# Performance work log

Measured on AMD Instinct MI355X. Metric: run time of the kernel, lower is better.

The kernel has to match this reference:

```python
import jax, jax.numpy as jnp
import numpy as np

B, S, D_IN, D_OUT = 4, 4096, 512, 512


def setup_inputs() -> dict:
    key = jax.random.key(0)
    k1, k2, k3, k4 = jax.random.split(key, 4)
    sc = 1.0 / np.sqrt(D_IN)
    return {
        "x": jax.random.normal(k1, (B, S, D_IN), dtype=jnp.float32),
        "Wq": jax.random.normal(k2, (D_OUT, D_IN), dtype=jnp.float32) * sc,
        "Wk": jax.random.normal(k3, (D_OUT, D_IN), dtype=jnp.float32) * sc,
        "Wv": jax.random.normal(k4, (D_OUT, D_IN), dtype=jnp.float32) * sc,
    }


def reference(x, Wq, Wk, Wv):
    # nn.Linear: y = x @ W.T  (no bias)
    q = jnp.einsum("bsd,ed->bse", x, Wq)  # [B,S,D_OUT]
    k = jnp.einsum("bsd,ed->bse", x, Wk)
    v = jnp.einsum("bsd,ed->bse", x, Wv)
    scale = 1.0 / jnp.sqrt(jnp.asarray(k.shape[-1], dtype=x.dtype))
    scores = jnp.einsum("bqe,bke->bqk", q, k) * scale  # [B,S,S]
    # causal mask: position q attends to k <= q
    s = x.shape[1]
    causal = jnp.tril(jnp.ones((s, s), dtype=bool))
    scores = jnp.where(causal[None, :, :], scores, -jnp.inf)
    attn = jax.nn.softmax(scores, axis=-1)
    # dropout p=0.0 -> identity
    return jnp.einsum("bqk,bke->bqe", attn, v)  # [B,S,D_OUT]
```

## Files before the change

kernel.cpp:

```cpp
#include <hip/hip_runtime.h>

typedef __attribute__((ext_vector_type(8))) short short8;
typedef __attribute__((ext_vector_type(4))) float f32x4;

#define GLD_AS1 const __attribute__((address_space(1))) void*
#define GLD_AS3 __attribute__((address_space(3))) void*

__device__ __forceinline__ unsigned short f2bf(float f) {
  unsigned u = __builtin_bit_cast(unsigned, f);
  u += 0x7fffu + ((u >> 16) & 1u);
  return (unsigned short)(u >> 16);
}
__device__ __forceinline__ float bf2f(unsigned short h) {
  return __builtin_bit_cast(float, (unsigned)h << 16);
}

__global__ void cvt_f32_bf16(const float* __restrict__ in, unsigned short* __restrict__ out, int n4) {
  int i = blockIdx.x * blockDim.x + threadIdx.x;
  const int st = gridDim.x * blockDim.x;
  for (; i < n4; i += st) {
    float4 f = reinterpret_cast<const float4*>(in)[i];
    unsigned long long p = (unsigned long long)f2bf(f.x)
        | ((unsigned long long)f2bf(f.y) << 16)
        | ((unsigned long long)f2bf(f.z) << 32)
        | ((unsigned long long)f2bf(f.w) << 48);
    reinterpret_cast<unsigned long long*>(out)[i] = p;
  }
}

__global__ void cvt_w3(const float* __restrict__ wq, const float* __restrict__ wk,
                       const float* __restrict__ wv, unsigned short* __restrict__ wcat) {
  const int n4 = 3 * 65536;
  int i = blockIdx.x * blockDim.x + threadIdx.x;
  const int st = gridDim.x * blockDim.x;
  for (; i < n4; i += st) {
    const int seg = i >> 16, off = i & 65535;
    const float* src = (seg == 0) ? wq : (seg == 1) ? wk : wv;
    float4 f = reinterpret_cast<const float4*>(src)[off];
    unsigned long long p = (unsigned long long)f2bf(f.x)
        | ((unsigned long long)f2bf(f.y) << 16)
        | ((unsigned long long)f2bf(f.z) << 32)
        | ((unsigned long long)f2bf(f.w) << 48);
    reinterpret_cast<unsigned long long*>(wcat)[i] = p;
  }
}

__global__ __launch_bounds__(256) void qkv_gemm(
    const unsigned short* __restrict__ xb, const unsigned short* __restrict__ wcat,
    unsigned short* __restrict__ qb, unsigned short* __restrict__ kb,
    unsigned short* __restrict__ vtb) {
  __shared__ unsigned short As[128 * 64];
  __shared__ unsigned short Bs[128 * 64];
  const int tid = threadIdx.x, lane = tid & 63, w = tid >> 6;
  const int m0 = blockIdx.y * 128, n0 = blockIdx.x * 128;
  const int wr = w >> 1, wc = w & 1;
  const float QSCALE = 0.0637587085f;

  f32x4 acc[4][4];
  const f32x4 z4 = {0.f, 0.f, 0.f, 0.f};
  #pragma unroll
  for (int a = 0; a < 4; ++a)
    #pragma unroll
    for (int c = 0; c < 4; ++c) acc[a][c] = z4;

  for (int it = 0; it < 8; ++it) {
    const int k0 = it * 64;
    #pragma unroll
    for (int c = 0; c < 4; ++c) {
      const int rbase = 32 * w + 8 * c;
      const int r = rbase + (lane >> 3);
      const int c16 = (lane & 7) ^ (r & 7);
      const unsigned short* ga = xb + (size_t)(m0 + r) * 512 + k0 + c16 * 8;
      const unsigned short* gb = wcat + (size_t)(n0 + r) * 512 + k0 + c16 * 8;
      __builtin_amdgcn_global_load_lds((GLD_AS1)ga, (GLD_AS3)&As[rbase * 64], 16, 0, 0);
      __builtin_amdgcn_global_load_lds((GLD_AS1)gb, (GLD_AS3)&Bs[rbase * 64], 16, 0, 0);
    }
    __syncthreads();
    #pragma unroll
    for (int ks = 0; ks < 2; ++ks) {
      const int ck = ks * 4 + (lane >> 4);
      short8 av[4], bv[4];
      #pragma unroll
      for (int fr = 0; fr < 4; ++fr) {
        const int rl = 64 * wr + 16 * fr + (lane & 15);
        av[fr] = *reinterpret_cast<const short8*>(&As[rl * 64 + ((ck ^ (rl & 7)) << 3)]);
      }
      #pragma unroll
      for (int fc = 0; fc < 4; ++fc) {
        const int rl = 64 * wc + 16 * fc + (lane & 15);
        bv[fc] = *reinterpret_cast<const short8*>(&Bs[rl * 64 + ((ck ^ (rl & 7)) << 3)]);
      }
      #pragma unroll
      for (int fr = 0; fr < 4; ++fr)
        #pragma unroll
        for (int fc = 0; fc < 4; ++fc)
          acc[fr][fc] = __builtin_amdgcn_mfma_f32_16x16x32_bf16(av[fr], bv[fc], acc[fr][fc], 0, 0, 0);
    }
    __syncthreads();
  }

  const int which = n0 >> 9;
  #pragma unroll
  for (int fr = 0; fr < 4; ++fr) {
    #pragma unroll
    for (int fc = 0; fc < 4; ++fc) {
      const int n = n0 + 64 * wc + 16 * fc + (lane & 15);
      const int nl = n & 511;
      #pragma unroll
      for (int j = 0; j < 4; ++j) {
        const int m = m0 + 64 * wr + 16 * fr + (lane >> 4) * 4 + j;
        const float a = acc[fr][fc][j];
        const unsigned short v = f2bf(which == 0 ? a * QSCALE : a);
        if (which == 0)      qb[(size_t)m * 512 + nl] = v;
        else if (which == 1) kb[(size_t)m * 512 + nl] = v;
        else                 vtb[((size_t)((m >> 12) * 512 + nl)) * 4096 + (m & 4095)] = v;
      }
    }
  }
}

#define FENCE() __builtin_amdgcn_sched_barrier(0)
#define BAR_VM8()  do { FENCE(); asm volatile("s_waitcnt vmcnt(8) lgkmcnt(0)" ::: "memory"); \
                        FENCE(); __builtin_amdgcn_s_barrier(); FENCE(); } while (0)
#define BAR_VM0()  do { FENCE(); asm volatile("s_waitcnt vmcnt(0) lgkmcnt(0)" ::: "memory"); \
                        FENCE(); __builtin_amdgcn_s_barrier(); FENCE(); } while (0)

__global__ __launch_bounds__(512, 2) void attn_fwd(
    const unsigned short* __restrict__ qg, const unsigned short* __restrict__ kg,
    const unsigned short* __restrict__ vtg,
    float* __restrict__ out0,
    unsigned short* __restrict__ out1,
    float* __restrict__ ml) {
  __shared__ __align__(16) unsigned short Ks[2][64 * 512];
  __shared__ __align__(16) unsigned short P_lds[2][64][72];
  __shared__ __align__(16) float psums[2][64];

  const int tid = threadIdx.x, lane = tid & 63, w = tid >> 6;
  const int idx = blockIdx.x;
  const int qt = 63 - (idx >> 3);
  const int b = (idx >> 1) & 3;
  const int half = idx & 1;
  const int nkt = qt + 1;
  const int kt0 = half ? (nkt >> 1) : 0;
  const int kt1 = half ? nkt : (nkt >> 1);
  const int q0 = qt * 64;

  const unsigned short* Qb  = qg  + (size_t)b * 4096 * 512;
  const unsigned short* Kb  = kg  + (size_t)b * 4096 * 512;
  const unsigned short* Vtb = vtg + (size_t)b * 512 * 4096;

  const int wr = w & 3, wc = w >> 2, g = lane >> 4, dw = w * 64;
  const int rbase = 16 * wr + 4 * g;

  short8 qreg[16];
  {
    const unsigned short* qrow = Qb + (size_t)(q0 + 16 * wr + (lane & 15)) * 512 + (lane >> 4) * 8;
    #pragma unroll
    for (int ks = 0; ks < 16; ++ks)
      qreg[ks] = *reinterpret_cast<const short8*>(qrow + ks * 32);
  }

  const f32x4 z4 = {0.f, 0.f, 0.f, 0.f};
  f32x4 oacc[4][4];
  #pragma unroll
  for (int fr = 0; fr < 4; ++fr)
    #pragma unroll
    for (int fc = 0; fc < 4; ++fc) oacc[fr][fc] = z4;

  float l_run[4];
  #pragma unroll
  for (int j = 0; j < 4; ++j) l_run[j] = 0.f;

  short8 vreg[2][4];
  f32x4 sacc_cur[2], sacc_nxt[2];

#define STAGE_K(kt_) do {                                                                \
    _Pragma("unroll")                                                                    \
    for (int r8 = 0; r8 < 8; ++r8) {                                                     \
      const int r_ = r8 * 8 + w;                                                         \
      const unsigned short* g_ = Kb + (size_t)((kt_) * 64 + r_) * 512 + (lane ^ (r_ & 7)) * 8; \
      __builtin_amdgcn_global_load_lds((GLD_AS1)g_, (GLD_AS3)&Ks[(kt_) & 1][r_ * 512], 16, 0, 0); \
    }                                                                                    \
  } while (0)

#define QK_TILE(buf_, S_) do {                                                           \
    _Pragma("unroll")                                                                    \
    for (int ks = 0; ks < 16; ++ks) {                                                    \
      const int ck = ks * 4 + (lane >> 4);                                               \
      _Pragma("unroll")                                                                  \
      for (int fc = 0; fc < 2; ++fc) {                                                   \
        const int rl = 32 * wc + 16 * fc + (lane & 15);                                  \
        const short8 bv = *reinterpret_cast<const short8*>(                              \
            &Ks[buf_][rl * 512 + ((ck ^ (rl & 7)) << 3)]);                               \
        S_[fc] = __builtin_amdgcn_mfma_f32_16x16x32_bf16(qreg[ks], bv, S_[fc], 0, 0, 0); \
      }                                                                                  \
    }                                                                                    \
  } while (0)

#define PV_STEP(pb_) do {                                                                \
    _Pragma("unroll")                                                                    \
    for (int ks = 0; ks < 2; ++ks) {                                                     \
      short8 av[4];                                                                      \
      _Pragma("unroll")                                                                  \
      for (int fr = 0; fr < 4; ++fr)                                                     \
        av[fr] = *reinterpret_cast<const short8*>(                                       \
            &P_lds[pb_][16 * fr + (lane & 15)][ks * 32 + (lane >> 4) * 8]);              \
      __builtin_amdgcn_s_setprio(1);                                                     \
      _Pragma("unroll")                                                                  \
      for (int fr = 0; fr < 4; ++fr)                                                     \
        _Pragma("unroll")                                                                \
        for (int fc = 0; fc < 4; ++fc)                                                   \
          oacc[fr][fc] = __builtin_amdgcn_mfma_f32_16x16x32_bf16(av[fr], vreg[ks][fc],   \
                                                                 oacc[fr][fc], 0, 0, 0);\
      __builtin_amdgcn_s_setprio(0);                                                     \
    }                                                                                    \
  } while (0)

  if (kt0 < kt1) {
    STAGE_K(kt0);
    const bool two = (kt0 + 1 < kt1);
    if (two) STAGE_K(kt0 + 1);
    FENCE();
    if (two) { asm volatile("s_waitcnt vmcnt(8)" ::: "memory"); }
    else     { asm volatile("s_waitcnt vmcnt(0)" ::: "memory"); }
    FENCE();
    __builtin_amdgcn_s_barrier();
    FENCE();
    sacc_cur[0] = z4; sacc_cur[1] = z4;
    QK_TILE(kt0 & 1, sacc_cur);
    BAR_VM0();

    for (int t = kt0; t < kt1; ++t) {
      if (t + 2 < kt1) STAGE_K(t + 2);
      FENCE();
      if (t > kt0) PV_STEP((t - 1) & 1);
      if (t == qt) {
        #pragma unroll
        for (int fc = 0; fc < 2; ++fc) {
          const int col = 32 * wc + 16 * fc + (lane & 15);
          #pragma unroll
          for (int j = 0; j < 4; ++j)
            if (col > rbase + j) sacc_cur[fc][j] = -1e30f;
        }
      }
      {
        const int colb = 32 * wc + (lane & 15);
        #pragma unroll
        for (int j = 0; j < 4; ++j) {
          const float p0 = __builtin_amdgcn_exp2f(sacc_cur[0][j]);
          const float p1 = __builtin_amdgcn_exp2f(sacc_cur[1][j]);
          l_run[j] += p0 + p1;
          P_lds[t & 1][rbase + j][colb]      = f2bf(p0);
          P_lds[t & 1][rbase + j][colb + 16] = f2bf(p1);
        }
      }
      const int kv0 = t * 64;
      #pragma unroll
      for (int ks = 0; ks < 2; ++ks)
        #pragma unroll
        for (int fc = 0; fc < 4; ++fc)
          vreg[ks][fc] = *reinterpret_cast<const short8*>(
              Vtb + (size_t)(dw + 16 * fc + (lane & 15)) * 4096 + kv0 + ks * 32 + (lane >> 4) * 8);
      if (t + 1 < kt1) {
        sacc_nxt[0] = z4; sacc_nxt[1] = z4;
        __builtin_amdgcn_s_setprio(1);
        QK_TILE((t + 1) & 1, sacc_nxt);
        __builtin_amdgcn_s_setprio(0);
        sacc_cur[0] = sacc_nxt[0]; sacc_cur[1] = sacc_nxt[1];
      }
      BAR_VM8();
    }
    PV_STEP((kt1 - 1) & 1);
  }

  #pragma unroll
  for (int j = 0; j < 4; ++j) {
    l_run[j] += __shfl_xor(l_run[j], 1);
    l_run[j] += __shfl_xor(l_run[j], 2);
    l_run[j] += __shfl_xor(l_run[j], 4);
    l_run[j] += __shfl_xor(l_run[j], 8);
  }
  if ((lane & 15) == 0) {
    f32x4 l4 = {l_run[0], l_run[1], l_run[2], l_run[3]};
    *reinterpret_cast<f32x4*>(&psums[wc][rbase]) = l4;
  }
  __syncthreads();
  if ((lane & 15) == 0 && wc == 0) {
    const int rg = b * 4096 + q0 + rbase;
    const f32x4 la = *reinterpret_cast<const f32x4*>(&psums[0][rbase]);
    const f32x4 lb = *reinterpret_cast<const f32x4*>(&psums[1][rbase]);
    f32x4 m4 = {0.f, 0.f, 0.f, 0.f};
    f32x4 l4 = {la[0] + lb[0], la[1] + lb[1], la[2] + lb[2], la[3] + lb[3]};
    *reinterpret_cast<f32x4*>(&ml[(half * 2) * 16384 + rg])     = m4;
    *reinterpret_cast<f32x4*>(&ml[(half * 2 + 1) * 16384 + rg]) = l4;
  }
  if (half == 0) {
    float* ob = out0 + (size_t)b * 4096 * 512;
    #pragma unroll
    for (int fr = 0; fr < 4; ++fr)
      #pragma unroll
      for (int j = 0; j < 4; ++j) {
        const int row = 16 * fr + (lane >> 4) * 4 + j;
        #pragma unroll
        for (int fc = 0; fc < 4; ++fc)
          ob[(size_t)(q0 + row) * 512 + dw + 16 * fc + (lane & 15)] = oacc[fr][fc][j];
      }
  } else {
    unsigned short* ob = out1 + (size_t)b * 4096 * 512;
    #pragma unroll
    for (int fr = 0; fr < 4; ++fr)
      #pragma unroll
      for (int j = 0; j < 4; ++j) {
        const int row = 16 * fr + (lane >> 4) * 4 + j;
        #pragma unroll
        for (int fc = 0; fc < 4; ++fc)
          ob[(size_t)(q0 + row) * 512 + dw + 16 * fc + (lane & 15)] = f2bf(oacc[fr][fc][j]);
      }
  }
#undef STAGE_K
#undef QK_TILE
#undef PV_STEP
}

__global__ void attn_merge(float* __restrict__ out, const unsigned short* __restrict__ o1,
                           const float* __restrict__ ml) {
  const int total = 16384 * 128;
  int i = blockIdx.x * blockDim.x + threadIdx.x;
  const int st = gridDim.x * blockDim.x;
  for (; i < total; i += st) {
    const int r = i >> 7;
    const float m0 = ml[r], l0 = ml[16384 + r];
    const float m1 = ml[2 * 16384 + r], l1 = ml[3 * 16384 + r];
    const float m = fmaxf(m0, m1);
    const float a0 = __builtin_amdgcn_exp2f(m0 - m), a1 = __builtin_amdgcn_exp2f(m1 - m);
    const float inv = 1.0f / (a0 * l0 + a1 * l1);
    const float s0 = a0 * inv, s1 = a1 * inv;
    float4 v0 = reinterpret_cast<const float4*>(out)[i];
    ushort4 v1 = reinterpret_cast<const ushort4*>(o1)[i];
    float4 o;
    o.x = v0.x * s0 + bf2f(v1.x) * s1;
    o.y = v0.y * s0 + bf2f(v1.y) * s1;
    o.z = v0.z * s0 + bf2f(v1.z) * s1;
    o.w = v0.w * s0 + bf2f(v1.w) * s1;
    reinterpret_cast<float4*>(out)[i] = o;
  }
}

extern "C" void kernel_launch(void* const* d_in, const int* in_sizes, int n_in,
                              void* d_out, int out_size, void* d_ws, size_t ws_size,
                              hipStream_t stream) {
  const float* x  = (const float*)d_in[0];
  const float* wq = (const float*)d_in[1];
  const float* wk = (const float*)d_in[2];
  const float* wv = (const float*)d_in[3];

  char* ws = (char*)d_ws;
  unsigned short* xb   = (unsigned short*)(ws);
  unsigned short* wcat = (unsigned short*)(ws + (16u << 20));
  float*          mlp  = (float*)(ws + (18u << 20));
  unsigned short* qb   = (unsigned short*)(ws + (20u << 20));
  unsigned short* kb   = (unsigned short*)(ws + (36u << 20));
  unsigned short* vtb  = (unsigned short*)(ws + (52u << 20));

  cvt_f32_bf16<<<2048, 256, 0, stream>>>(x, xb, (4 * 4096 * 512) / 4);
  cvt_w3<<<768, 256, 0, stream>>>(wq, wk, wv, wcat);

  qkv_gemm<<<dim3(12, 128), 256, 0, stream>>>(xb, wcat, qb, kb, vtb);

  attn_fwd<<<512, 512, 0, stream>>>(qb, kb, vtb, (float*)d_out, xb, mlp);
  attn_merge<<<2048, 256, 0, stream>>>((float*)d_out, xb, mlp);
}
```

Before: 203.8 us.

## Fuse x bf16 conversion into QKV GEMM and read K directly from global

Drops the separate f32-to-bf16 conversion kernel for x. The QKV GEMM now loads fp32 x, converts it in registers and writes it to the swizzled LDS tile, which removes one launch and one bf16 round trip of x. Separately, the attention kernel no longer stages K tiles into a double-buffered 64 KB LDS buffer and reads K fragments straight from global/L2 inside QK_TILE. That frees LDS and barrier/wait overhead, but the K loads are now uncoalesced, unswizzled and unpipelined, which may stall the MFMA loop.

```diff
diff --git a/kernel.cpp b/kernel.cpp
--- a/kernel.cpp
+++ b/kernel.cpp
@@ -13,19 +13,6 @@
 }
 __device__ __forceinline__ float bf2f(unsigned short h) {
   return __builtin_bit_cast(float, (unsigned)h << 16);
-}
-
-__global__ void cvt_f32_bf16(const float* __restrict__ in, unsigned short* __restrict__ out, int n4) {
-  int i = blockIdx.x * blockDim.x + threadIdx.x;
-  const int st = gridDim.x * blockDim.x;
-  for (; i < n4; i += st) {
-    float4 f = reinterpret_cast<const float4*>(in)[i];
-    unsigned long long p = (unsigned long long)f2bf(f.x)
-        | ((unsigned long long)f2bf(f.y) << 16)
-        | ((unsigned long long)f2bf(f.z) << 32)
-        | ((unsigned long long)f2bf(f.w) << 48);
-    reinterpret_cast<unsigned long long*>(out)[i] = p;
-  }
 }
 
 __global__ void cvt_w3(const float* __restrict__ wq, const float* __restrict__ wk,
@@ -46,7 +33,7 @@
 }
 
 __global__ __launch_bounds__(256) void qkv_gemm(
-    const unsigned short* __restrict__ xb, const unsigned short* __restrict__ wcat,
+    const float* __restrict__ x, const unsigned short* __restrict__ wcat,
     unsigned short* __restrict__ qb, unsigned short* __restrict__ kb,
     unsigned short* __restrict__ vtb) {
   __shared__ unsigned short As[128 * 64];
@@ -70,10 +57,22 @@
       const int rbase = 32 * w + 8 * c;
       const int r = rbase + (lane >> 3);
       const int c16 = (lane & 7) ^ (r & 7);
-      const unsigned short* ga = xb + (size_t)(m0 + r) * 512 + k0 + c16 * 8;
       const unsigned short* gb = wcat + (size_t)(n0 + r) * 512 + k0 + c16 * 8;
-      __builtin_amdgcn_global_load_lds((GLD_AS1)ga, (GLD_AS3)&As[rbase * 64], 16, 0, 0);
       __builtin_amdgcn_global_load_lds((GLD_AS1)gb, (GLD_AS3)&Bs[rbase * 64], 16, 0, 0);
+    }
+    #pragma unroll
+    for (int i = 0; i < 4; ++i) {
+      const int cid = tid + 256 * i;
+      const int r = cid >> 3, c = cid & 7;
+      const float* src = &x[(size_t)(m0 + r) * 512 + k0 + c * 8];
+      const float4 f0 = *reinterpret_cast<const float4*>(src);
+      const float4 f1 = *reinterpret_cast<const float4*>(src + 4);
+      short8 v;
+      v[0] = (short)f2bf(f0.x); v[1] = (short)f2bf(f0.y);
+      v[2] = (short)f2bf(f0.z); v[3] = (short)f2bf(f0.w);
+      v[4] = (short)f2bf(f1.x); v[5] = (short)f2bf(f1.y);
+      v[6] = (short)f2bf(f1.z); v[7] = (short)f2bf(f1.w);
+      *reinterpret_cast<short8*>(&As[r * 64 + ((c ^ (r & 7)) << 3)]) = v;
     }
     __syncthreads();
     #pragma unroll
@@ -120,10 +119,6 @@
 }
 
 #define FENCE() __builtin_amdgcn_sched_barrier(0)
-#define BAR_VM8()  do { FENCE(); asm volatile("s_waitcnt vmcnt(8) lgkmcnt(0)" ::: "memory"); \
-                        FENCE(); __builtin_amdgcn_s_barrier(); FENCE(); } while (0)
-#define BAR_VM0()  do { FENCE(); asm volatile("s_waitcnt vmcnt(0) lgkmcnt(0)" ::: "memory"); \
-                        FENCE(); __builtin_amdgcn_s_barrier(); FENCE(); } while (0)
 
 __global__ __launch_bounds__(512, 2) void attn_fwd(
     const unsigned short* __restrict__ qg, const unsigned short* __restrict__ kg,
@@ -131,7 +126,6 @@
     float* __restrict__ out0,
     unsigned short* __restrict__ out1,
     float* __restrict__ ml) {
-  __shared__ __align__(16) unsigned short Ks[2][64 * 512];
   __shared__ __align__(16) unsigned short P_lds[2][64][72];
   __shared__ __align__(16) float psums[2][64];
 
@@ -174,16 +168,7 @@
   short8 vreg[2][4];
   f32x4 sacc_cur[2], sacc_nxt[2];
 
-#define STAGE_K(kt_) do {                                                                \
-    _Pragma("unroll")                                                                    \
-    for (int r8 = 0; r8 < 8; ++r8) {                                                     \
-      const int r_ = r8 * 8 + w;                                                         \
-      const unsigned short* g_ = Kb + (size_t)((kt_) * 64 + r_) * 512 + (lane ^ (r_ & 7)) * 8; \
-      __builtin_amdgcn_global_load_lds((GLD_AS1)g_, (GLD_AS3)&Ks[(kt_) & 1][r_ * 512], 16, 0, 0); \
-    }                                                                                    \
-  } while (0)
-
-#define QK_TILE(buf_, S_) do {                                                           \
+#define QK_TILE(kv0_, S_) do {                                                           \
     _Pragma("unroll")                                                                    \
     for (int ks = 0; ks < 16; ++ks) {                                                    \
       const int ck = ks * 4 + (lane >> 4);                                               \
@@ -191,7 +176,7 @@
       for (int fc = 0; fc < 2; ++fc) {                                                   \
         const int rl = 32 * wc + 16 * fc + (lane & 15);                                  \
         const short8 bv = *reinterpret_cast<const short8*>(                              \
-            &Ks[buf_][rl * 512 + ((ck ^ (rl & 7)) << 3)]);                               \
+            Kb + (size_t)((kv0_) + rl) * 512 + ck * 8);                                  \
         S_[fc] = __builtin_amdgcn_mfma_f32_16x16x32_bf16(qreg[ks], bv, S_[fc], 0, 0, 0); \
       }                                                                                  \
     }                                                                                    \
@@ -217,22 +202,10 @@
   } while (0)
 
   if (kt0 < kt1) {
-    STAGE_K(kt0);
-    const bool two = (kt0 + 1 < kt1);
-    if (two) STAGE_K(kt0 + 1);
-    FENCE();
-    if (two) { asm volatile("s_waitcnt vmcnt(8)" ::: "memory"); }
-    else     { asm volatile("s_waitcnt vmcnt(0)" ::: "memory"); }
-    FENCE();
-    __builtin_amdgcn_s_barrier();
-    FENCE();
     sacc_cur[0] = z4; sacc_cur[1] = z4;
-    QK_TILE(kt0 & 1, sacc_cur);
-    BAR_VM0();
+    QK_TILE(kt0 * 64, sacc_cur);
 
     for (int t = kt0; t < kt1; ++t) {
-      if (t + 2 < kt1) STAGE_K(t + 2);
-      FENCE();
       if (t > kt0) PV_STEP((t - 1) & 1);
       if (t == qt) {
         #pragma unroll
@@ -264,11 +237,15 @@
       if (t + 1 < kt1) {
         sacc_nxt[0] = z4; sacc_nxt[1] = z4;
         __builtin_amdgcn_s_setprio(1);
-        QK_TILE((t + 1) & 1, sacc_nxt);
+        QK_TILE((t + 1) * 64, sacc_nxt);
         __builtin_amdgcn_s_setprio(0);
         sacc_cur[0] = sacc_nxt[0]; sacc_cur[1] = sacc_nxt[1];
       }
-      BAR_VM8();
+      FENCE();
+      asm volatile("s_waitcnt lgkmcnt(0)" ::: "memory");
+      FENCE();
+      __builtin_amdgcn_s_barrier();
+      FENCE();
     }
     PV_STEP((kt1 - 1) & 1);
   }
@@ -317,7 +294,6 @@
           ob[(size_t)(q0 + row) * 512 + dw + 16 * fc + (lane & 15)] = f2bf(oacc[fr][fc][j]);
       }
   }
-#undef STAGE_K
 #undef QK_TILE
 #undef PV_STEP
 }
@@ -355,18 +331,17 @@
   const float* wv = (const float*)d_in[3];
 
   char* ws = (char*)d_ws;
-  unsigned short* xb   = (unsigned short*)(ws);
+  unsigned short* o1b  = (unsigned short*)(ws);
   unsigned short* wcat = (unsigned short*)(ws + (16u << 20));
   float*          mlp  = (float*)(ws + (18u << 20));
   unsigned short* qb   = (unsigned short*)(ws + (20u << 20));
   unsigned short* kb   = (unsigned short*)(ws + (36u << 20));
   unsigned short* vtb  = (unsigned short*)(ws + (52u << 20));
 
-  cvt_f32_bf16<<<2048, 256, 0, stream>>>(x, xb, (4 * 4096 * 512) / 4);
   cvt_w3<<<768, 256, 0, stream>>>(wq, wk, wv, wcat);
 
-  qkv_gemm<<<dim3(12, 128), 256, 0, stream>>>(xb, wcat, qb, kb, vtb);
-
-  attn_fwd<<<512, 512, 0, stream>>>(qb, kb, vtb, (float*)d_out, xb, mlp);
-  attn_merge<<<2048, 256, 0, stream>>>((float*)d_out, xb, mlp);
-}
+  qkv_gemm<<<dim3(12, 128), 256, 0, stream>>>(x, wcat, qb, kb, vtb);
+
+  attn_fwd<<<512, 512, 0, stream>>>(qb, kb, vtb, (float*)d_out, o1b, mlp);
+  attn_merge<<<2048, 256, 0, stream>>>((float*)d_out, o1b, mlp);
+}
```

Result: slower. 428.6 us (+110.3%).
